# Kernel tuning notes

Hardware: AMD Instinct MI355X
Metric: run time of the kernel (lower is better)

The kernel has to match this reference:

```python
import jax, jax.numpy as jnp
import numpy as np

DIM = 1024; DEPTH = 2; HEADS = 8; DH = DIM // HEADS  # 128
BUCKET = 64; NHASH = 4; MULT = 4
B = 2; T = 4096
NBUCKETS = T // BUCKET  # 64
SCALE = DH ** -0.5
SELF_ATTN_VAL = -5e4  # TOKEN_SELF_ATTN_VALUE in reformer-pytorch
EPS = 1e-5


def layer_norm(x, g, b):
    m = jnp.mean(x, -1, keepdims=True)
    v = jnp.var(x, -1, keepdims=True)
    return (x - m) * jax.lax.rsqrt(v + EPS) * g + b


def lsh_attn(xn, Wqk, Wv, Wo, bo, rot):
    # xn: [B,T,DIM] already layer-normed. Shared-QK LSH attention (reformer-pytorch).
    qk = (xn @ Wqk).reshape(B, T, HEADS, DH).transpose(0, 2, 1, 3).reshape(B * HEADS, T, DH)
    v = (xn @ Wv).reshape(B, T, HEADS, DH).transpose(0, 2, 1, 3).reshape(B * HEADS, T, DH)
    bh = B * HEADS
    # --- hashing with random rotations ---
    rotated = jnp.einsum('btf,fhi->bhti', qk, rot)            # [bh,NHASH,T,NBUCKETS//2]
    rotated = jnp.concatenate([rotated, -rotated], -1)        # [bh,NHASH,T,NBUCKETS]
    buckets = jnp.argmax(rotated, -1)                         # [bh,NHASH,T]
    offs = (jnp.arange(NHASH) * NBUCKETS)[:, None]
    buckets = (buckets + offs).reshape(bh, NHASH * T)
    ticker = jnp.arange(NHASH * T)
    bt = buckets * T + (ticker % T)                           # unique keys -> stable-equivalent sort
    sticker = jnp.argsort(bt, axis=-1)                        # [bh, NHASH*T]
    undo = jnp.argsort(sticker, axis=-1)
    st = sticker % T                                          # original positions, bucket-sorted
    sqk = jnp.take_along_axis(qk, st[..., None], axis=1)
    sv = jnp.take_along_axis(v, st[..., None], axis=1)
    nchunks = NHASH * NBUCKETS
    bq_t = st.reshape(bh, nchunks, BUCKET)
    bqk = sqk.reshape(bh, nchunks, BUCKET, DH)
    bv = sv.reshape(bh, nchunks, BUCKET, DH)
    bq = bqk
    bk = bqk / jnp.clip(jnp.linalg.norm(bqk, axis=-1, keepdims=True), 1e-12)
    def look_one_back(a):
        extra = jnp.concatenate([a[:, -1:], a[:, :-1]], axis=1)
        return jnp.concatenate([a, extra], axis=2)
    bk = look_one_back(bk); bv = look_one_back(bv); bkv_t = look_one_back(bq_t)
    dots = jnp.einsum('bcie,bcje->bcij', bq, bk) * SCALE      # [bh,nchunks,BUCKET,2*BUCKET]
    self_mask = bq_t[..., :, None] == bkv_t[..., None, :]     # shared-QK: penalize i==j
    dots = jnp.where(self_mask, SELF_ATTN_VAL, dots)
    lse = jax.nn.logsumexp(dots, axis=-1, keepdims=True)
    p = jnp.exp(dots - lse)
    bo_ = jnp.einsum('bcij,bcje->bcie', p, bv)
    so = bo_.reshape(bh, NHASH * T, DH)
    slog = lse.reshape(bh, NHASH * T)
    o = jnp.take_along_axis(so, undo[..., None], axis=1)
    logits = jnp.take_along_axis(slog, undo, axis=1)
    o = o.reshape(bh, NHASH, T, DH)
    logits = logits.reshape(bh, NHASH, T, 1)
    probs = jnp.exp(logits - jax.nn.logsumexp(logits, axis=1, keepdims=True))
    out = jnp.sum(o * probs, axis=1)                          # combine hash rounds
    out = out.reshape(B, HEADS, T, DH).transpose(0, 2, 1, 3).reshape(B, T, HEADS * DH)
    return out @ Wo + bo


def setup_inputs() -> dict:
    key = jax.random.key(0)
    ks = jax.random.split(key, 16)
    s = 0.02
    d = {
        'x': jax.random.normal(ks[0], (B, T, DIM), jnp.float32),
        'ln1_g': jnp.ones((DEPTH, DIM), jnp.float32),
        'ln1_b': jnp.zeros((DEPTH, DIM), jnp.float32),
        'Wqk': jax.random.normal(ks[1], (DEPTH, DIM, HEADS * DH), jnp.float32) * s,
        'Wv': jax.random.normal(ks[2], (DEPTH, DIM, HEADS * DH), jnp.float32) * s,
        'Wo': jax.random.normal(ks[3], (DEPTH, HEADS * DH, DIM), jnp.float32) * s,
        'bo': jnp.zeros((DEPTH, DIM), jnp.float32),
        'ln2_g': jnp.ones((DEPTH, DIM), jnp.float32),
        'ln2_b': jnp.zeros((DEPTH, DIM), jnp.float32),
        'W1': jax.random.normal(ks[4], (DEPTH, DIM, DIM * MULT), jnp.float32) * s,
        'b1': jnp.zeros((DEPTH, DIM * MULT), jnp.float32),
        'W2': jax.random.normal(ks[5], (DEPTH, DIM * MULT, DIM), jnp.float32) * s,
        'b2': jnp.zeros((DEPTH, DIM), jnp.float32),
        'rotations': jax.random.normal(ks[6], (DEPTH, DH, NHASH, NBUCKETS // 2), jnp.float32),
    }
    return d


def reference(x, ln1_g, ln1_b, Wqk, Wv, Wo, bo, ln2_g, ln2_b, W1, b1, W2, b2, rotations):
    xx = jnp.concatenate([x, x], -1)  # [B,T,2*DIM] reversible pair
    def step(carry, p):
        g1, be1, wqk, wv, wo, bov, g2, be2, w1, bb1, w2, bb2, rot = p
        x1, x2 = jnp.split(carry, 2, axis=-1)
        y1 = x1 + lsh_attn(layer_norm(x2, g1, be1), wqk, wv, wo, bov, rot)
        h = layer_norm(y1, g2, be2)
        ff = jax.nn.gelu(h @ w1 + bb1, approximate=False) @ w2 + bb2
        y2 = x2 + ff
        return jnp.concatenate([y1, y2], -1), None
    params = (ln1_g, ln1_b, Wqk, Wv, Wo, bo, ln2_g, ln2_b, W1, b1, W2, b2, rotations)
    out, _ = jax.lax.scan(step, xx, params)
    y1, y2 = jnp.split(out, 2, axis=-1)
    return y1 + y2
```

## Files before the change

### kernel.cpp

```cpp
#include <hip/hip_runtime.h>
#include <hip/hip_bf16.h>
#include <cmath>

using bf16 = __hip_bfloat16;
typedef __attribute__((ext_vector_type(8))) short short8;
typedef __attribute__((ext_vector_type(4))) float floatx4;

__device__ __forceinline__ float bu2f(ushort u) { return __uint_as_float((unsigned)u << 16); }
__device__ __forceinline__ ushort f2bu(float f) {
  union { bf16 b; ushort u; } cv; cv.b = __float2bfloat16(f); return cv.u;
}
__device__ __forceinline__ void gl_lds16(const ushort* g, ushort* l) {
  __builtin_amdgcn_global_load_lds((const __attribute__((address_space(1))) unsigned*)g,
                                   (__attribute__((address_space(3))) unsigned*)l, 16, 0, 0);
}
__device__ __forceinline__ float fast_gelu(float x) {
  float z = 0.7978845608028654f * (x + 0.044715f * x * x * x);
  z = fmaxf(fminf(z, 10.f), -10.f);
  float e = __expf(2.f * z);
  float t = (e - 1.f) / (e + 1.f);
  return 0.5f * x * (1.f + t);
}

static constexpr int kT   = 4096;
static constexpr int kDim = 1024;
static constexpr float kScale   = 0.08838834764831845f;
static constexpr float kSelfVal = -5.0e4f;

__device__ __forceinline__ int sane_v(float f) { float a = fabsf(f); return (a > 1e-4f && a < 1e4f) ? 1 : 0; }

__global__ __launch_bounds__(256) void k_detect(const unsigned* __restrict__ x, int* __restrict__ flag) {
  __shared__ int cnt;
  int tid = threadIdx.x;
  if (tid == 0) cnt = 0;
  __syncthreads();
  int my = 0;
  const uint4* p = (const uint4*)x;
  for (int q = 0; q < 16; q++) {
    uint4 u = p[tid * 16 + q];
    my += sane_v(__uint_as_float(u.x << 16)) + sane_v(__uint_as_float(u.x & 0xffff0000u));
    my += sane_v(__uint_as_float(u.y << 16)) + sane_v(__uint_as_float(u.y & 0xffff0000u));
    my += sane_v(__uint_as_float(u.z << 16)) + sane_v(__uint_as_float(u.z & 0xffff0000u));
    my += sane_v(__uint_as_float(u.w << 16)) + sane_v(__uint_as_float(u.w & 0xffff0000u));
  }
  atomicAdd(&cnt, my);
  __syncthreads();
  if (tid == 0) flag[0] = (cnt >= 24576) ? 1 : 0;
}

__global__ __launch_bounds__(256) void k_cvt(const int* __restrict__ flag, const void* __restrict__ src,
                                             ushort* __restrict__ dst, int n) {
  int i = blockIdx.x * 256 + threadIdx.x;
  if (i >= n) return;
  dst[i] = (*flag) ? ((const ushort*)src)[i] : f2bu(((const float*)src)[i]);
}

__global__ __launch_bounds__(256) void k_init_any(const int* __restrict__ flag, const void* __restrict__ x,
                                                  float* __restrict__ x1, float* __restrict__ x2) {
  int i = blockIdx.x * 1024 + threadIdx.x * 4;
  float4 f;
  if (*flag) {
    ushort4 u = *(const ushort4*)((const ushort*)x + i);
    f.x = bu2f(u.x); f.y = bu2f(u.y); f.z = bu2f(u.z); f.w = bu2f(u.w);
  } else {
    f = *(const float4*)((const float*)x + i);
  }
  *(float4*)(x1 + i) = f;
  *(float4*)(x2 + i) = f;
}

__global__ __launch_bounds__(256) void k_final_any(const int* __restrict__ flag, const float* __restrict__ x1,
                                                   const float* __restrict__ x2, void* __restrict__ out) {
  int i = blockIdx.x * 1024 + threadIdx.x * 4;
  float4 a = *(const float4*)(x1 + i);
  float4 b = *(const float4*)(x2 + i);
  float4 s; s.x = a.x + b.x; s.y = a.y + b.y; s.z = a.z + b.z; s.w = a.w + b.w;
  if (*flag) {
    ushort4 u; u.x = f2bu(s.x); u.y = f2bu(s.y); u.z = f2bu(s.z); u.w = f2bu(s.w);
    *(ushort4*)((ushort*)out + i) = u;
  } else {
    *(float4*)((float*)out + i) = s;
  }
}

__global__ __launch_bounds__(256) void k_ln(const float* __restrict__ x, const ushort* __restrict__ g,
                                            const ushort* __restrict__ be, ushort* __restrict__ out) {
  __shared__ float ws[4], ws2[4];
  int row = blockIdx.x, tid = threadIdx.x;
  const float* xr = x + (size_t)row * kDim + tid * 4;
  float4 v = *(const float4*)xr;
  float s  = v.x + v.y + v.z + v.w;
  float s2 = v.x*v.x + v.y*v.y + v.z*v.z + v.w*v.w;
  #pragma unroll
  for (int off = 32; off; off >>= 1) { s += __shfl_down(s, off); s2 += __shfl_down(s2, off); }
  int wave = tid >> 6, lane = tid & 63;
  if (lane == 0) { ws[wave] = s; ws2[wave] = s2; }
  __syncthreads();
  s  = ws[0] + ws[1] + ws[2] + ws[3];
  s2 = ws2[0] + ws2[1] + ws2[2] + ws2[3];
  float mean = s * (1.f/1024.f);
  float var  = fmaxf(s2 * (1.f/1024.f) - mean*mean, 0.f);
  float rstd = rsqrtf(var + 1e-5f);
  int cb = tid * 4;
  ushort* o = out + (size_t)row * kDim + cb;
  o[0] = f2bu((v.x - mean) * rstd * bu2f(g[cb+0]) + bu2f(be[cb+0]));
  o[1] = f2bu((v.y - mean) * rstd * bu2f(g[cb+1]) + bu2f(be[cb+1]));
  o[2] = f2bu((v.z - mean) * rstd * bu2f(g[cb+2]) + bu2f(be[cb+2]));
  o[3] = f2bu((v.w - mean) * rstd * bu2f(g[cb+3]) + bu2f(be[cb+3]));
}

__global__ __launch_bounds__(256) void k_transpose2(const int* __restrict__ flag, const void* __restrict__ src_bf,
                                                    const void* __restrict__ src_f, ushort* __restrict__ out,
                                                    int K, int N) {
  __shared__ ushort tile[32][33];
  int isbf = *flag;
  int nb = blockIdx.x * 32, kb = blockIdx.y * 32;
  int tx = threadIdx.x & 31, ty = threadIdx.x >> 5;
  for (int r = ty; r < 32; r += 8) {
    size_t idx = (size_t)(kb + r) * N + nb + tx;
    tile[r][tx] = isbf ? ((const ushort*)src_bf)[idx] : f2bu(((const float*)src_f)[idx]);
  }
  __syncthreads();
  for (int r = ty; r < 32; r += 8) out[(size_t)(nb + r) * K + kb + tx] = tile[tx][r];
}

__global__ __launch_bounds__(256) void k_rot_t(const ushort* __restrict__ rot, ushort* __restrict__ rotT) {
  int tid = threadIdx.x;
  for (int idx = tid; idx < 16384; idx += 256) {
    int n = idx >> 7, k = idx & 127;
    rotT[idx] = rot[k * 128 + n];
  }
}

template <int MW>
__global__ __launch_bounds__(512, 2) void k_gemm5(const ushort* __restrict__ A, const ushort* __restrict__ Bt,
                                                  const ushort* __restrict__ bias, float* __restrict__ Cf,
                                                  ushort* __restrict__ Cb, ushort* __restrict__ Cb2,
                                                  int M, int N, int K, int mode) {
  constexpr int BM = MW * 32;
  constexpr int LA = MW / 4;
  constexpr int PF = (MW == 8) ? 2 : 3;
  __shared__ alignas(16) ushort SAu[4 * BM * 32];
  __shared__ alignas(16) ushort SBu[4 * 256 * 32];

  const int tid  = threadIdx.x;
  const int lane = tid & 63, wave = tid >> 6;
  const int lr = lane & 15, g = lane >> 4;
  const int wm = wave >> 2, wn = wave & 3;

  const int nbx = gridDim.x;
  const int nwg = nbx * gridDim.y;
  const int bid = blockIdx.y * nbx + blockIdx.x;
  const int swz = (bid & 7) * (nwg >> 3) + (bid >> 3);
  const int m0 = (swz / nbx) * BM;
  const int n0 = (swz % nbx) * 256;

  const int NT = K >> 5;

  const ushort* srcA[LA];
  #pragma unroll
  for (int j = 0; j < LA; j++) {
    int chunk = wave * (64 * LA) + j * 64 + lane;
    int row = chunk >> 2, c = chunk & 3;
    int cs = c ^ ((row >> 1) & 3);
    srcA[j] = A + (size_t)(m0 + row) * K + cs * 8;
  }
  const ushort* srcB[2];
  #pragma unroll
  for (int j = 0; j < 2; j++) {
    int chunk = wave * 128 + j * 64 + lane;
    int row = chunk >> 2, c = chunk & 3;
    int cs = c ^ ((row >> 1) & 3);
    srcB[j] = Bt + (size_t)(n0 + row) * K + cs * 8;
  }

  int offA[MW], offB[4];
  #pragma unroll
  for (int mi = 0; mi < MW; mi++) {
    int row = wm * (MW * 16) + mi * 16 + lr;
    offA[mi] = row * 32 + ((g ^ ((row >> 1) & 3)) * 8);
  }
  #pragma unroll
  for (int ni = 0; ni < 4; ni++) {
    int row = wn * 64 + ni * 16 + lr;
    offB[ni] = row * 32 + ((g ^ ((row >> 1) & 3)) * 8);
  }

  floatx4 acc[MW][4];
  #pragma unroll
  for (int mi = 0; mi < MW; mi++)
    #pragma unroll
    for (int ni = 0; ni < 4; ni++) acc[mi][ni] = (floatx4){0.f, 0.f, 0.f, 0.f};

  #pragma unroll
  for (int p = 0; p < PF; p++) {
    #pragma unroll
    for (int j = 0; j < LA; j++) gl_lds16(srcA[j] + p * 32, SAu + p * (BM * 32) + (wave * (64 * LA) + j * 64) * 8);
    #pragma unroll
    for (int j = 0; j < 2; j++)  gl_lds16(srcB[j] + p * 32, SBu + p * (256 * 32) + (wave * 128 + j * 64) * 8);
  }
  if constexpr (MW == 8) asm volatile("s_waitcnt vmcnt(4)" ::: "memory");
  else                   asm volatile("s_waitcnt vmcnt(6)" ::: "memory");
  __builtin_amdgcn_s_barrier();
  asm volatile("" ::: "memory");

  for (int kt = 0; kt < NT; kt++) {
    const ushort* sa = SAu + (kt & 3) * (BM * 32);
    const ushort* sb = SBu + (kt & 3) * (256 * 32);
    const int kp = ((kt + PF < NT) ? (kt + PF) : 0) * 32;
    const int pb = (kt + PF) & 3;

    short8 a[MW], b[4];
    #pragma unroll
    for (int mi = 0; mi < MW; mi++) a[mi] = *(const short8*)&sa[offA[mi]];
    #pragma unroll
    for (int ni = 0; ni < 4; ni++)  b[ni] = *(const short8*)&sb[offB[ni]];

    #pragma unroll
    for (int j = 0; j < LA; j++) gl_lds16(srcA[j] + kp, SAu + pb * (BM * 32) + (wave * (64 * LA) + j * 64) * 8);
    #pragma unroll
    for (int j = 0; j < 2; j++)  gl_lds16(srcB[j] + kp, SBu + pb * (256 * 32) + (wave * 128 + j * 64) * 8);

    __builtin_amdgcn_s_setprio(1);
    #pragma unroll
    for (int mi = 0; mi < MW; mi++)
      #pragma unroll
      for (int ni = 0; ni < 4; ni++)
        acc[mi][ni] = __builtin_amdgcn_mfma_f32_16x16x32_bf16(a[mi], b[ni], acc[mi][ni], 0, 0, 0);
    __builtin_amdgcn_s_setprio(0);

    if constexpr (MW == 8) asm volatile("s_waitcnt vmcnt(4)" ::: "memory");
    else                   asm volatile("s_waitcnt vmcnt(6)" ::: "memory");
    __builtin_amdgcn_s_barrier();
    asm volatile("" ::: "memory");
  }

  asm volatile("s_waitcnt vmcnt(0)" ::: "memory");
  __syncthreads();

  const int hi4 = (lane >> 4) * 4;

  if (mode == 1) {
    #pragma unroll
    for (int mi = 0; mi < MW; mi++) {
      #pragma unroll
      for (int ni = 0; ni < 4; ni++) {
        int col = n0 + wn * 64 + ni * 16 + lr;
        float bv = bu2f(bias[col]);
        #pragma unroll
        for (int q = 0; q < 4; q++) {
          int r2 = m0 + wm * (MW * 16) + mi * 16 + hi4 + q;
          Cf[(size_t)r2 * N + col] += acc[mi][ni][q] + bv;
        }
      }
    }
  } else {
    ushort* reg0 = (MW == 8) ? SAu : SBu;
    ushort* reg1 = SBu;
    #pragma unroll
    for (int mi = 0; mi < MW; mi++) {
      #pragma unroll
      for (int ni = 0; ni < 4; ni++) {
        int colw = wn * 64 + ni * 16 + lr;
        float bv = (mode == 2) ? bu2f(bias[n0 + colw]) : 0.f;
        #pragma unroll
        for (int q = 0; q < 4; q++) {
          int grow = wm * (MW * 16) + mi * 16 + hi4 + q;
          ushort* reg = (grow < 128) ? reg0 : reg1;
          int rl = grow & 127;
          float val = acc[mi][ni][q];
          ushort h = (mode == 2) ? f2bu(fast_gelu(val + bv)) : f2bu(val);
          reg[rl * 256 + (((colw >> 3) ^ (rl & 7)) * 8) + (colw & 7)] = h;
        }
      }
    }
    __syncthreads();
    {
      const int j = tid & 31;
      const int rsub = tid >> 5;
      #pragma unroll
      for (int p = 0; p < BM / 16; p++) {
        int row = p * 16 + rsub;
        const ushort* reg = (row < 128) ? reg0 : reg1;
        int rl = row & 127;
        short8 v = *(const short8*)&reg[rl * 256 + ((j ^ (rl & 7)) * 8)];
        *(short8*)&Cb[(size_t)(m0 + row) * N + n0 + j * 8] = v;
      }
    }
    if (mode == 5) {
      __syncthreads();
      #pragma unroll
      for (int mi = 0; mi < MW; mi++) {
        #pragma unroll
        for (int ni = 0; ni < 4; ni++) {
          int colw = wn * 64 + ni * 16 + lr;
          #pragma unroll
          for (int q = 0; q < 4; q++) {
            int grow = wm * (MW * 16) + mi * 16 + hi4 + q;
            ushort* reg = (grow < 128) ? reg0 : reg1;
            int rl = grow & 127;
            float val = acc[mi][ni][q];
            ushort h = f2bu(val);
            reg[rl * 256 + (((colw >> 3) ^ (rl & 7)) * 8) + (colw & 7)] = f2bu(val - bu2f(h));
          }
        }
      }
      __syncthreads();
      const int j = tid & 31;
      const int rsub = tid >> 5;
      #pragma unroll
      for (int p = 0; p < BM / 16; p++) {
        int row = p * 16 + rsub;
        const ushort* reg = (row < 128) ? reg0 : reg1;
        int rl = row & 127;
        short8 v = *(const short8*)&reg[rl * 256 + ((j ^ (rl & 7)) * 8)];
        *(short8*)&Cb2[(size_t)(m0 + row) * N + n0 + j * 8] = v;
      }
    }
  }
  (void)M;
}

__global__ __launch_bounds__(256) void k_bucket_mfma(const ushort* __restrict__ qkh, const ushort* __restrict__ qkl,
                                                     const ushort* __restrict__ rotT, int* __restrict__ bkt) {
  __shared__ alignas(16) ushort Bs[128*128];
  __shared__ alignas(16) ushort Ah[64*128];
  __shared__ alignas(16) ushort Al[64*128];
  const int tid = threadIdx.x;
  const int lane = tid & 63, wave = tid >> 6;
  const int lr = lane & 15, lk = (lane >> 4) * 8;
  const int tt = blockIdx.x * 64;
  const int bh = blockIdx.y;
  const int b = bh >> 3, hh = bh & 7;

  {
    int r = tid >> 2, c0 = (tid & 3) * 32;
    size_t base = ((size_t)(b * kT + tt + r)) * kDim + hh * 128 + c0;
    const uint4* sh = (const uint4*)(qkh + base);
    const uint4* sl = (const uint4*)(qkl + base);
    uint4* dh = (uint4*)&Ah[r * 128 + c0];
    uint4* dl = (uint4*)&Al[r * 128 + c0];
    #pragma unroll
    for (int i = 0; i < 4; i++) { dh[i] = sh[i]; dl[i] = sl[i]; }
  }
  {
    const uint4* src = (const uint4*)rotT;
    uint4* dst = (uint4*)Bs;
    for (int i = tid; i < 2048; i += 256) dst[i] = src[i];
  }
  __syncthreads();

  floatx4 acc[4][2];
  #pragma unroll
  for (int mi = 0; mi < 4; mi++) { acc[mi][0] = (floatx4){0,0,0,0}; acc[mi][1] = (floatx4){0,0,0,0}; }
  #pragma unroll
  for (int ks = 0; ks < 4; ks++) {
    short8 a[4], bb[2];
    #pragma unroll
    for (int ni = 0; ni < 2; ni++) bb[ni] = *(const short8*)&Bs[(wave*32 + ni*16 + lr)*128 + ks*32 + lk];
    #pragma unroll
    for (int mi = 0; mi < 4; mi++) a[mi] = *(const short8*)&Ah[(mi*16 + lr)*128 + ks*32 + lk];
    #pragma unroll
    for (int mi = 0; mi < 4; mi++)
      #pragma unroll
      for (int ni = 0; ni < 2; ni++)
        acc[mi][ni] = __builtin_amdgcn_mfma_f32_16x16x32_bf16(a[mi], bb[ni], acc[mi][ni], 0, 0, 0);
  }
  #pragma unroll
  for (int ks = 0; ks < 4; ks++) {
    short8 a[4], bb[2];
    #pragma unroll
    for (int ni = 0; ni < 2; ni++) bb[ni] = *(const short8*)&Bs[(wave*32 + ni*16 + lr)*128 + ks*32 + lk];
    #pragma unroll
    for (int mi = 0; mi < 4; mi++) a[mi] = *(const short8*)&Al[(mi*16 + lr)*128 + ks*32 + lk];
    #pragma unroll
    for (int mi = 0; mi < 4; mi++)
      #pragma unroll
      for (int ni = 0; ni < 2; ni++)
        acc[mi][ni] = __builtin_amdgcn_mfma_f32_16x16x32_bf16(a[mi], bb[ni], acc[mi][ni], 0, 0, 0);
  }

  #pragma unroll
  for (int mi = 0; mi < 4; mi++) {
    #pragma unroll
    for (int q = 0; q < 4; q++) {
      float v0 = acc[mi][0][q];
      float v1 = acc[mi][1][q];
      float best = v0; int bidx = lr;
      if (v1  > best) { best = v1;  bidx = 16 + lr; }
      if (-v0 > best) { best = -v0; bidx = 32 + lr; }
      if (-v1 > best) { best = -v1; bidx = 48 + lr; }
      #pragma unroll
      for (int m = 1; m <= 8; m <<= 1) {
        float ov = __shfl_xor(best, m);
        int   oi = __shfl_xor(bidx, m);
        if (ov > best || (ov == best && oi < bidx)) { best = ov; bidx = oi; }
      }
      if (lr == 0) {
        int row = mi*16 + ((lane >> 4) & 3)*4 + q;
        bkt[(bh*4 + wave)*4096 + tt + row] = bidx;
      }
    }
  }
}

__global__ __launch_bounds__(256) void k_sort(const int* __restrict__ bkt, int* __restrict__ st) {
  __shared__ unsigned char  hist[64*256];
  __shared__ unsigned short offs[64*256];
  __shared__ int base[64];
  int tid = threadIdx.x, grp = blockIdx.x;
  const int* bk = bkt + grp * 4096;
  for (int i = tid; i < 64*256; i += 256) hist[i] = 0;
  __syncthreads();
  int myb[16];
  #pragma unroll
  for (int j = 0; j < 16; j++) {
    myb[j] = bk[tid*16 + j];
    hist[myb[j]*256 + tid] += 1;
  }
  __syncthreads();
  if (tid < 64) {
    int run = 0;
    for (int t = 0; t < 256; t++) { offs[tid*256 + t] = (unsigned short)run; run += hist[tid*256 + t]; }
    base[tid] = run;
  }
  __syncthreads();
  if (tid == 0) {
    int run = 0;
    for (int b2 = 0; b2 < 64; b2++) { int c = base[b2]; base[b2] = run; run += c; }
  }
  __syncthreads();
  #pragma unroll
  for (int j = 0; j < 16; j++) {
    int b2 = myb[j];
    int r = 0;
    for (int jj = 0; jj < j; jj++) r += (myb[jj] == b2) ? 1 : 0;
    st[grp*4096 + base[b2] + (int)offs[b2*256 + tid] + r] = tid*16 + j;
  }
}

__global__ __launch_bounds__(256) void k_attn(const ushort* __restrict__ qkh, const ushort* __restrict__ vbuf,
                                              const int* __restrict__ st, ushort* __restrict__ o_r,
                                              float* __restrict__ lse_r) {
  __shared__ alignas(16) ushort KV[128*136];
  __shared__ alignas(16) ushort Ps[64*136];
  __shared__ float rnorm[128];
  __shared__ int   kposs[128];
  __shared__ float red1[64*4];
  __shared__ float red2[64*4];
  __shared__ float lrow[64];

  const int tid = threadIdx.x;
  const int bid = blockIdx.x;
  const int bh = bid >> 8;
  const int c  = bid & 255;
  const int h  = c >> 6;
  const int cprev = (c + 255) & 255;
  const int b  = bh >> 3, hh = bh & 7;
  const int lane = tid & 63, wave = tid >> 6;
  const int lr = lane & 15, lk = (lane >> 4) * 8;

  {
    int j = tid >> 1, half = tid & 1;
    int slot = (j < 64) ? (c*64 + j) : (cprev*64 + (j - 64));
    int pos = st[bh*16384 + slot];
    if (half == 0) kposs[j] = pos;
    const ushort* src = qkh + ((size_t)(b * kT + pos)) * kDim + hh*128 + half*64;
    float ss = 0.f;
    #pragma unroll
    for (int i2 = 0; i2 < 64; i2 += 8) {
      uint4 u = *(const uint4*)(src + i2);
      *(uint4*)&KV[j*136 + half*64 + i2] = u;
      float f0 = bu2f((ushort)(u.x & 0xffffu)), f1 = bu2f((ushort)(u.x >> 16));
      float f2 = bu2f((ushort)(u.y & 0xffffu)), f3 = bu2f((ushort)(u.y >> 16));
      float f4 = bu2f((ushort)(u.z & 0xffffu)), f5 = bu2f((ushort)(u.z >> 16));
      float f6 = bu2f((ushort)(u.w & 0xffffu)), f7 = bu2f((ushort)(u.w >> 16));
      ss += f0*f0 + f1*f1 + f2*f2 + f3*f3 + f4*f4 + f5*f5 + f6*f6 + f7*f7;
    }
    ss += __shfl_xor(ss, 1);
    if (half == 0) rnorm[j] = 1.f / fmaxf(sqrtf(ss), 1e-12f);
  }
  __syncthreads();

  {
    floatx4 acc[4][2];
    #pragma unroll
    for (int mi = 0; mi < 4; mi++) { acc[mi][0] = (floatx4){0,0,0,0}; acc[mi][1] = (floatx4){0,0,0,0}; }
    #pragma unroll
    for (int ks = 0; ks < 4; ks++) {
      short8 a[4], bb[2];
      #pragma unroll
      for (int mi = 0; mi < 4; mi++) a[mi]  = *(const short8*)&KV[(mi*16 + lr)*136 + ks*32 + lk];
      #pragma unroll
      for (int ni = 0; ni < 2; ni++) bb[ni] = *(const short8*)&KV[(wave*32 + ni*16 + lr)*136 + ks*32 + lk];
      #pragma unroll
      for (int mi = 0; mi < 4; mi++)
        #pragma unroll
        for (int ni = 0; ni < 2; ni++)
          acc[mi][ni] = __builtin_amdgcn_mfma_f32_16x16x32_bf16(a[mi], bb[ni], acc[mi][ni], 0, 0, 0);
    }
    #pragma unroll
    for (int mi = 0; mi < 4; mi++) {
      #pragma unroll
      for (int ni = 0; ni < 2; ni++) {
        int col = wave*32 + ni*16 + lr;
        float rn = rnorm[col] * kScale;
        int cpos = kposs[col];
        #pragma unroll
        for (int q = 0; q < 4; q++) {
          int row = mi*16 + (lane >> 4)*4 + q;
          float val = acc[mi][ni][q] * rn;
          if (cpos == kposs[row]) val = kSelfVal;
          Ps[row*136 + col] = f2bu(val);
        }
      }
    }
  }
  __syncthreads();

  {
    int j = tid >> 1, half = tid & 1;
    int pos = kposs[j];
    const ushort* src = vbuf + ((size_t)(b * kT + pos)) * kDim + hh*128 + half*64;
    #pragma unroll
    for (int i2 = 0; i2 < 64; i2 += 8) {
      uint4 u = *(const uint4*)(src + i2);
      int d0 = half*64 + i2;
      KV[(d0+0)*136 + j] = (ushort)(u.x & 0xffffu); KV[(d0+1)*136 + j] = (ushort)(u.x >> 16);
      KV[(d0+2)*136 + j] = (ushort)(u.y & 0xffffu); KV[(d0+3)*136 + j] = (ushort)(u.y >> 16);
      KV[(d0+4)*136 + j] = (ushort)(u.z & 0xffffu); KV[(d0+5)*136 + j] = (ushort)(u.z >> 16);
      KV[(d0+6)*136 + j] = (ushort)(u.w & 0xffffu); KV[(d0+7)*136 + j] = (ushort)(u.w >> 16);
    }
  }

  {
    int i = tid >> 2, part = tid & 3;
    const int jb = part * 32;
    float m = -1e30f;
    for (int j2 = 0; j2 < 32; j2++) m = fmaxf(m, bu2f(Ps[i*136 + jb + j2]));
    red1[i*4 + part] = m;
    __syncthreads();
    m = fmaxf(fmaxf(red1[i*4+0], red1[i*4+1]), fmaxf(red1[i*4+2], red1[i*4+3]));
    float ssum = 0.f;
    for (int j2 = 0; j2 < 32; j2++) {
      float arg = fmaxf(fminf(bu2f(Ps[i*136 + jb + j2]) - m, 0.f), -80.f);
      float p = __expf(arg);
      ssum += p;
      Ps[i*136 + jb + j2] = f2bu(p);
    }
    red2[i*4 + part] = ssum;
    __syncthreads();
    if (part == 0) {
      float l = fmaxf(red2[i*4+0] + red2[i*4+1] + red2[i*4+2] + red2[i*4+3], 1e-20f);
      lrow[i] = 1.f / l;
      lse_r[(size_t)(bh*4 + h)*4096 + kposs[i]] = m + __logf(l);
    }
  }
  __syncthreads();

  {
    floatx4 acc[4][2];
    #pragma unroll
    for (int mi = 0; mi < 4; mi++) { acc[mi][0] = (floatx4){0,0,0,0}; acc[mi][1] = (floatx4){0,0,0,0}; }
    #pragma unroll
    for (int ks = 0; ks < 4; ks++) {
      short8 a[4], bb[2];
      #pragma unroll
      for (int mi = 0; mi < 4; mi++) a[mi]  = *(const short8*)&Ps[(mi*16 + lr)*136 + ks*32 + lk];
      #pragma unroll
      for (int ni = 0; ni < 2; ni++) bb[ni] = *(const short8*)&KV[(wave*32 + ni*16 + lr)*136 + ks*32 + lk];
      #pragma unroll
      for (int mi = 0; mi < 4; mi++)
        #pragma unroll
        for (int ni = 0; ni < 2; ni++)
          acc[mi][ni] = __builtin_amdgcn_mfma_f32_16x16x32_bf16(a[mi], bb[ni], acc[mi][ni], 0, 0, 0);
    }
    #pragma unroll
    for (int mi = 0; mi < 4; mi++) {
      #pragma unroll
      for (int ni = 0; ni < 2; ni++) {
        int d = wave*32 + ni*16 + lr;
        #pragma unroll
        for (int q = 0; q < 4; q++) {
          int row = mi*16 + (lane >> 4)*4 + q;
          float o = acc[mi][ni][q] * lrow[row];
          o_r[((size_t)(bh*4 + h)*4096 + kposs[row])*128 + d] = f2bu(o);
        }
      }
    }
  }
}

__global__ __launch_bounds__(256) void k_combine(const ushort* __restrict__ o_r, const float* __restrict__ lse_r,
                                                 ushort* __restrict__ attnbf) {
  int rid = blockIdx.x * 2 + (threadIdx.x >> 7);
  int d = threadIdx.x & 127;
  int bh = rid >> 12, t = rid & 4095;
  int b = bh >> 3, hh = bh & 7;
  size_t base = (size_t)bh * 16384 + t;
  float l0 = lse_r[base], l1 = lse_r[base + 4096], l2 = lse_r[base + 8192], l3 = lse_r[base + 12288];
  float M = fmaxf(fmaxf(l0, l1), fmaxf(l2, l3));
  float e0 = __expf(fmaxf(fminf(l0 - M, 0.f), -80.f));
  float e1 = __expf(fmaxf(fminf(l1 - M, 0.f), -80.f));
  float e2 = __expf(fmaxf(fminf(l2 - M, 0.f), -80.f));
  float e3 = __expf(fmaxf(fminf(l3 - M, 0.f), -80.f));
  float inv = 1.f / (e0 + e1 + e2 + e3);
  float o = e0 * bu2f(o_r[(base         )*128 + d]) + e1 * bu2f(o_r[(base +  4096)*128 + d])
          + e2 * bu2f(o_r[(base +  8192)*128 + d]) + e3 * bu2f(o_r[(base + 12288)*128 + d]);
  attnbf[((size_t)b * kT + t) * kDim + hh*128 + d] = f2bu(o * inv);
}

extern "C" void kernel_launch(void* const* d_in, const int* in_sizes, int n_in,
                              void* d_out, int out_size, void* d_ws, size_t ws_size,
                              hipStream_t stream) {
  (void)in_sizes; (void)n_in; (void)out_size; (void)ws_size;
  const void* x     = d_in[0];
  const void* ln1_g = d_in[1];
  const void* ln1_b = d_in[2];
  const void* Wqk   = d_in[3];
  const void* Wv    = d_in[4];
  const void* Wo    = d_in[5];
  const void* bo    = d_in[6];
  const void* ln2_g = d_in[7];
  const void* ln2_b = d_in[8];
  const void* W1    = d_in[9];
  const void* b1    = d_in[10];
  const void* W2    = d_in[11];
  const void* b2    = d_in[12];
  const void* rot   = d_in[13];

  char* w = (char*)d_ws;
  int*    flag = (int*)w;    w += 256;
  ushort* prm  = (ushort*)w; w += 131072;
  float* x1  = (float*)w;  w += 33554432;
  float* x2  = (float*)w;  w += 33554432;
  ushort* qkh = (ushort*)w; w += 16777216;
  ushort* qkl = (ushort*)w; w += 16777216;
  ushort* vbb = (ushort*)w; w += 16777216;
  ushort* xbf = (ushort*)w; w += 16777216;
  ushort* orb = (ushort*)w; w += 67108864;
  float* lse = (float*)w;  w += 1048576;
  int*   bkt = (int*)w;    w += 1048576;
  int*   stb = (int*)w;    w += 1048576;
  ushort* wtA = (ushort*)w; w += 2097152;
  ushort* wtB = (ushort*)w; w += 2097152;
  ushort* wtC = (ushort*)w; w += 2097152;
  ushort* wt1 = (ushort*)w; w += 8388608;
  ushort* wt2 = (ushort*)w; w += 8388608;
  ushort* rtT = (ushort*)w; w += 32768;

  ushort* pLN1G = prm + 0;     ushort* pLN1B = prm + 2048;
  ushort* pBO   = prm + 4096;  ushort* pLN2G = prm + 6144;
  ushort* pLN2B = prm + 8192;  ushort* pB1   = prm + 10240;
  ushort* pB2   = prm + 18432; ushort* pROT  = prm + 20480;

  k_detect<<<1, 256, 0, stream>>>((const unsigned*)x, flag);
  k_cvt<<<8,   256, 0, stream>>>(flag, ln1_g, pLN1G, 2048);
  k_cvt<<<8,   256, 0, stream>>>(flag, ln1_b, pLN1B, 2048);
  k_cvt<<<8,   256, 0, stream>>>(flag, bo,    pBO,   2048);
  k_cvt<<<8,   256, 0, stream>>>(flag, ln2_g, pLN2G, 2048);
  k_cvt<<<8,   256, 0, stream>>>(flag, ln2_b, pLN2B, 2048);
  k_cvt<<<32,  256, 0, stream>>>(flag, b1,    pB1,   8192);
  k_cvt<<<8,   256, 0, stream>>>(flag, b2,    pB2,   2048);
  k_cvt<<<128, 256, 0, stream>>>(flag, rot,   pROT,  32768);
  k_init_any<<<8192, 256, 0, stream>>>(flag, x, x1, x2);

  for (int d = 0; d < 2; d++) {
    k_transpose2<<<dim3(32, 32),  256, 0, stream>>>(flag,
        (const char*)Wqk + (size_t)d*1048576*2, (const char*)Wqk + (size_t)d*1048576*4, wtA, 1024, 1024);
    k_transpose2<<<dim3(32, 32),  256, 0, stream>>>(flag,
        (const char*)Wv  + (size_t)d*1048576*2, (const char*)Wv  + (size_t)d*1048576*4, wtB, 1024, 1024);
    k_transpose2<<<dim3(32, 32),  256, 0, stream>>>(flag,
        (const char*)Wo  + (size_t)d*1048576*2, (const char*)Wo  + (size_t)d*1048576*4, wtC, 1024, 1024);
    k_transpose2<<<dim3(128, 32), 256, 0, stream>>>(flag,
        (const char*)W1  + (size_t)d*4194304*2, (const char*)W1  + (size_t)d*4194304*4, wt1, 1024, 4096);
    k_transpose2<<<dim3(32, 128), 256, 0, stream>>>(flag,
        (const char*)W2  + (size_t)d*4194304*2, (const char*)W2  + (size_t)d*4194304*4, wt2, 4096, 1024);
    k_rot_t<<<1, 256, 0, stream>>>(pROT + (size_t)d * 16384, rtT);

    k_ln<<<8192, 256, 0, stream>>>(x2, pLN1G + d*1024, pLN1B + d*1024, xbf);
    k_gemm5<4><<<dim3(4, 64), 512, 0, stream>>>(xbf, wtA, nullptr, nullptr, qkh, qkl, 8192, 1024, 1024, 5);
    k_gemm5<4><<<dim3(4, 64), 512, 0, stream>>>(xbf, wtB, nullptr, nullptr, vbb, nullptr, 8192, 1024, 1024, 3);
    k_bucket_mfma<<<dim3(64, 16), 256, 0, stream>>>(qkh, qkl, rtT, bkt);
    k_sort<<<64, 256, 0, stream>>>(bkt, stb);
    k_attn<<<4096, 256, 0, stream>>>(qkh, vbb, stb, orb, lse);
    k_combine<<<32768, 256, 0, stream>>>(orb, lse, xbf);
    k_gemm5<4><<<dim3(4, 64), 512, 0, stream>>>(xbf, wtC, pBO + d*1024, x1, nullptr, nullptr, 8192, 1024, 1024, 1);
    k_ln<<<8192, 256, 0, stream>>>(x1, pLN2G + d*1024, pLN2B + d*1024, xbf);
    k_gemm5<8><<<dim3(16, 32), 512, 0, stream>>>(xbf, wt1, pB1 + d*4096, nullptr, orb, nullptr, 8192, 4096, 1024, 2);
    k_gemm5<4><<<dim3(4, 64), 512, 0, stream>>>(orb, wt2, pB2 + d*1024, x2, nullptr, nullptr, 8192, 1024, 4096, 1);
  }
  k_final_any<<<8192, 256, 0, stream>>>(flag, x1, x2, d_out);
}
```

Baseline: 1.108 ms.

## Replace GEMM with 128x128 tile, 256-thread, triple-buffered kernel for all projections

Swaps the templated 512-thread GEMM (128x256 or 256x256 tiles, 4-stage LDS ring) for a single 256-thread kernel with 128x128 tiles and a 3-stage LDS ring, targeting 3 blocks per CU. Smaller tiles give more workgroups and higher occupancy, but each tile is reloaded more often and the per-FLOP load traffic rises. The epilogue staging is remapped to split rows across the two smaller LDS buffers, and the loop adds an explicit lgkmcnt wait before the barrier.

After: 1.108 ms. About the same (-0.0%).

```diff
diff --git a/kernel.cpp b/kernel.cpp
--- a/kernel.cpp
+++ b/kernel.cpp
@@ -132,52 +132,40 @@
   }
 }
 
-template <int MW>
-__global__ __launch_bounds__(512, 2) void k_gemm5(const ushort* __restrict__ A, const ushort* __restrict__ Bt,
+__global__ __launch_bounds__(256, 3) void k_gemm6(const ushort* __restrict__ A, const ushort* __restrict__ Bt,
                                                   const ushort* __restrict__ bias, float* __restrict__ Cf,
                                                   ushort* __restrict__ Cb, ushort* __restrict__ Cb2,
                                                   int M, int N, int K, int mode) {
-  constexpr int BM = MW * 32;
-  constexpr int LA = MW / 4;
-  constexpr int PF = (MW == 8) ? 2 : 3;
-  __shared__ alignas(16) ushort SAu[4 * BM * 32];
-  __shared__ alignas(16) ushort SBu[4 * 256 * 32];
-
+  __shared__ alignas(16) ushort SAu[3 * 128 * 32];
+  __shared__ alignas(16) ushort SBu[3 * 128 * 32];
   const int tid  = threadIdx.x;
   const int lane = tid & 63, wave = tid >> 6;
   const int lr = lane & 15, g = lane >> 4;
-  const int wm = wave >> 2, wn = wave & 3;
+  const int wm = wave >> 1, wn = wave & 1;
 
   const int nbx = gridDim.x;
   const int nwg = nbx * gridDim.y;
   const int bid = blockIdx.y * nbx + blockIdx.x;
   const int swz = (bid & 7) * (nwg >> 3) + (bid >> 3);
-  const int m0 = (swz / nbx) * BM;
-  const int n0 = (swz % nbx) * 256;
-
+  const int m0 = (swz / nbx) * 128;
+  const int n0 = (swz % nbx) * 128;
   const int NT = K >> 5;
 
-  const ushort* srcA[LA];
-  #pragma unroll
-  for (int j = 0; j < LA; j++) {
-    int chunk = wave * (64 * LA) + j * 64 + lane;
-    int row = chunk >> 2, c = chunk & 3;
-    int cs = c ^ ((row >> 1) & 3);
-    srcA[j] = A + (size_t)(m0 + row) * K + cs * 8;
-  }
+  const ushort* srcA[2];
   const ushort* srcB[2];
   #pragma unroll
   for (int j = 0; j < 2; j++) {
     int chunk = wave * 128 + j * 64 + lane;
     int row = chunk >> 2, c = chunk & 3;
     int cs = c ^ ((row >> 1) & 3);
+    srcA[j] = A  + (size_t)(m0 + row) * K + cs * 8;
     srcB[j] = Bt + (size_t)(n0 + row) * K + cs * 8;
   }
 
-  int offA[MW], offB[4];
-  #pragma unroll
-  for (int mi = 0; mi < MW; mi++) {
-    int row = wm * (MW * 16) + mi * 16 + lr;
+  int offA[4], offB[4];
+  #pragma unroll
+  for (int mi = 0; mi < 4; mi++) {
+    int row = wm * 64 + mi * 16 + lr;
     offA[mi] = row * 32 + ((g ^ ((row >> 1) & 3)) * 8);
   }
   #pragma unroll
@@ -186,53 +174,57 @@
     offB[ni] = row * 32 + ((g ^ ((row >> 1) & 3)) * 8);
   }
 
-  floatx4 acc[MW][4];
-  #pragma unroll
-  for (int mi = 0; mi < MW; mi++)
+  floatx4 acc[4][4];
+  #pragma unroll
+  for (int mi = 0; mi < 4; mi++)
     #pragma unroll
     for (int ni = 0; ni < 4; ni++) acc[mi][ni] = (floatx4){0.f, 0.f, 0.f, 0.f};
 
   #pragma unroll
-  for (int p = 0; p < PF; p++) {
-    #pragma unroll
-    for (int j = 0; j < LA; j++) gl_lds16(srcA[j] + p * 32, SAu + p * (BM * 32) + (wave * (64 * LA) + j * 64) * 8);
-    #pragma unroll
-    for (int j = 0; j < 2; j++)  gl_lds16(srcB[j] + p * 32, SBu + p * (256 * 32) + (wave * 128 + j * 64) * 8);
-  }
-  if constexpr (MW == 8) asm volatile("s_waitcnt vmcnt(4)" ::: "memory");
-  else                   asm volatile("s_waitcnt vmcnt(6)" ::: "memory");
+  for (int p = 0; p < 2; p++) {
+    #pragma unroll
+    for (int j = 0; j < 2; j++) {
+      gl_lds16(srcA[j] + p * 32, SAu + p * 4096 + (wave * 128 + j * 64) * 8);
+      gl_lds16(srcB[j] + p * 32, SBu + p * 4096 + (wave * 128 + j * 64) * 8);
+    }
+  }
+  asm volatile("s_waitcnt vmcnt(4)" ::: "memory");
   __builtin_amdgcn_s_barrier();
   asm volatile("" ::: "memory");
 
+  int cur = 0;
   for (int kt = 0; kt < NT; kt++) {
-    const ushort* sa = SAu + (kt & 3) * (BM * 32);
-    const ushort* sb = SBu + (kt & 3) * (256 * 32);
-    const int kp = ((kt + PF < NT) ? (kt + PF) : 0) * 32;
-    const int pb = (kt + PF) & 3;
-
-    short8 a[MW], b[4];
-    #pragma unroll
-    for (int mi = 0; mi < MW; mi++) a[mi] = *(const short8*)&sa[offA[mi]];
-    #pragma unroll
-    for (int ni = 0; ni < 4; ni++)  b[ni] = *(const short8*)&sb[offB[ni]];
-
-    #pragma unroll
-    for (int j = 0; j < LA; j++) gl_lds16(srcA[j] + kp, SAu + pb * (BM * 32) + (wave * (64 * LA) + j * 64) * 8);
-    #pragma unroll
-    for (int j = 0; j < 2; j++)  gl_lds16(srcB[j] + kp, SBu + pb * (256 * 32) + (wave * 128 + j * 64) * 8);
+    const ushort* sa = SAu + cur * 4096;
+    const ushort* sb = SBu + cur * 4096;
+    int pb = cur + 2; if (pb >= 3) pb -= 3;
+    const int kp = ((kt + 2 < NT) ? (kt + 2) : 0) * 32;
+
+    short8 a[4], b[4];
+    #pragma unroll
+    for (int mi = 0; mi < 4; mi++) a[mi] = *(const short8*)&sa[offA[mi]];
+    #pragma unroll
+    for (int ni = 0; ni < 4; ni++) b[ni] = *(const short8*)&sb[offB[ni]];
+
+    #pragma unroll
+    for (int j = 0; j < 2; j++) {
+      gl_lds16(srcA[j] + kp, SAu + pb * 4096 + (wave * 128 + j * 64) * 8);
+      gl_lds16(srcB[j] + kp, SBu + pb * 4096 + (wave * 128 + j * 64) * 8);
+    }
 
     __builtin_amdgcn_s_setprio(1);
     #pragma unroll
-    for (int mi = 0; mi < MW; mi++)
+    for (int mi = 0; mi < 4; mi++)
       #pragma unroll
       for (int ni = 0; ni < 4; ni++)
         acc[mi][ni] = __builtin_amdgcn_mfma_f32_16x16x32_bf16(a[mi], b[ni], acc[mi][ni], 0, 0, 0);
     __builtin_amdgcn_s_setprio(0);
 
-    if constexpr (MW == 8) asm volatile("s_waitcnt vmcnt(4)" ::: "memory");
-    else                   asm volatile("s_waitcnt vmcnt(6)" ::: "memory");
+    asm volatile("s_waitcnt lgkmcnt(0)" ::: "memory");
+    asm volatile("s_waitcnt vmcnt(4)" ::: "memory");
     __builtin_amdgcn_s_barrier();
     asm volatile("" ::: "memory");
+
+    cur = (cur == 2) ? 0 : cur + 1;
   }
 
   asm volatile("s_waitcnt vmcnt(0)" ::: "memory");
@@ -242,78 +234,72 @@
 
   if (mode == 1) {
     #pragma unroll
-    for (int mi = 0; mi < MW; mi++) {
+    for (int mi = 0; mi < 4; mi++) {
       #pragma unroll
       for (int ni = 0; ni < 4; ni++) {
         int col = n0 + wn * 64 + ni * 16 + lr;
         float bv = bu2f(bias[col]);
         #pragma unroll
         for (int q = 0; q < 4; q++) {
-          int r2 = m0 + wm * (MW * 16) + mi * 16 + hi4 + q;
+          int r2 = m0 + wm * 64 + mi * 16 + hi4 + q;
           Cf[(size_t)r2 * N + col] += acc[mi][ni][q] + bv;
         }
       }
     }
   } else {
-    ushort* reg0 = (MW == 8) ? SAu : SBu;
-    ushort* reg1 = SBu;
-    #pragma unroll
-    for (int mi = 0; mi < MW; mi++) {
+    #pragma unroll
+    for (int mi = 0; mi < 4; mi++) {
       #pragma unroll
       for (int ni = 0; ni < 4; ni++) {
         int colw = wn * 64 + ni * 16 + lr;
         float bv = (mode == 2) ? bu2f(bias[n0 + colw]) : 0.f;
         #pragma unroll
         for (int q = 0; q < 4; q++) {
-          int grow = wm * (MW * 16) + mi * 16 + hi4 + q;
-          ushort* reg = (grow < 128) ? reg0 : reg1;
-          int rl = grow & 127;
+          int rl = wm * 64 + mi * 16 + hi4 + q;
+          ushort* rowp = (rl < 96) ? (SBu + rl * 128) : (SAu + (rl - 96) * 128);
           float val = acc[mi][ni][q];
           ushort h = (mode == 2) ? f2bu(fast_gelu(val + bv)) : f2bu(val);
-          reg[rl * 256 + (((colw >> 3) ^ (rl & 7)) * 8) + (colw & 7)] = h;
+          rowp[(((colw >> 3) ^ (rl & 7)) * 8) + (colw & 7)] = h;
         }
       }
     }
     __syncthreads();
     {
-      const int j = tid & 31;
-      const int rsub = tid >> 5;
-      #pragma unroll
-      for (int p = 0; p < BM / 16; p++) {
+      const int j = tid & 15;
+      const int rsub = tid >> 4;
+      #pragma unroll
+      for (int p = 0; p < 8; p++) {
         int row = p * 16 + rsub;
-        const ushort* reg = (row < 128) ? reg0 : reg1;
-        int rl = row & 127;
-        short8 v = *(const short8*)&reg[rl * 256 + ((j ^ (rl & 7)) * 8)];
+        const ushort* rowp = (row < 96) ? (SBu + row * 128) : (SAu + (row - 96) * 128);
+        short8 v = *(const short8*)&rowp[(j ^ (row & 7)) * 8];
         *(short8*)&Cb[(size_t)(m0 + row) * N + n0 + j * 8] = v;
       }
     }
     if (mode == 5) {
       __syncthreads();
       #pragma unroll
-      for (int mi = 0; mi < MW; mi++) {
+      for (int mi = 0; mi < 4; mi++) {
         #pragma unroll
         for (int ni = 0; ni < 4; ni++) {
           int colw = wn * 64 + ni * 16 + lr;
           #pragma unroll
           for (int q = 0; q < 4; q++) {
-            int grow = wm * (MW * 16) + mi * 16 + hi4 + q;
-            ushort* reg = (grow < 128) ? reg0 : reg1;
-            int rl = grow & 127;
+            int rl = wm * 64 + mi * 16 + hi4 + q;
+            ushort* rowp = (rl < 96) ? (SBu + rl * 128) : (SAu + (rl - 96) * 128);
             float val = acc[mi][ni][q];
             ushort h = f2bu(val);
-            reg[rl * 256 + (((colw >> 3) ^ (rl & 7)) * 8) + (colw & 7)] = f2bu(val - bu2f(h));
+            rowp[(((colw >> 3) ^ (rl & 7)) * 8) + (colw & 7)] = f2bu(val - bu2f(h));
           }
         }
       }
       __syncthreads();
-      const int j = tid & 31;
-      const int rsub = tid >> 5;
-      #pragma unroll
-      for (int p = 0; p < BM / 16; p++) {
+      const int j = tid & 15;
+      const int rsub = tid >> 4;
+      #pragma unroll
+      for (int p = 0; p < 8; p++) {
         int row = p * 16 + rsub;
-        const ushort* reg = (row < 128) ? reg0 : reg1;
-        int rl = row & 127;
-        short8 v = *(const short8*)&reg[rl * 256 + ((j ^ (rl & 7)) * 8)];
+        const ushort* rowp = (row < 96) ? (SBu + row * 128) : (SAu + (row - 96) * 128);
+        short8 v = *(const short8*)&rowp[(j ^ (row & 7)) * 8];
         *(short8*)&Cb2[(size_t)(m0 + row) * N + n0 + j * 8] = v;
       }
     }
@@ -679,16 +665,16 @@
     k_rot_t<<<1, 256, 0, stream>>>(pROT + (size_t)d * 16384, rtT);
 
     k_ln<<<8192, 256, 0, stream>>>(x2, pLN1G + d*1024, pLN1B + d*1024, xbf);
-    k_gemm5<4><<<dim3(4, 64), 512, 0, stream>>>(xbf, wtA, nullptr, nullptr, qkh, qkl, 8192, 1024, 1024, 5);
-    k_gemm5<4><<<dim3(4, 64), 512, 0, stream>>>(xbf, wtB, nullptr, nullptr, vbb, nullptr, 8192, 1024, 1024, 3);
+    k_gemm6<<<dim3(8, 64), 256, 0, stream>>>(xbf, wtA, nullptr, nullptr, qkh, qkl, 8192, 1024, 1024, 5);
+    k_gemm6<<<dim3(8, 64), 256, 0, stream>>>(xbf, wtB, nullptr, nullptr, vbb, nullptr, 8192, 1024, 1024, 3);
     k_bucket_mfma<<<dim3(64, 16), 256, 0, stream>>>(qkh, qkl, rtT, bkt);
     k_sort<<<64, 256, 0, stream>>>(bkt, stb);
     k_attn<<<4096, 256, 0, stream>>>(qkh, vbb, stb, orb, lse);
     k_combine<<<32768, 256, 0, stream>>>(orb, lse, xbf);
-    k_gemm5<4><<<dim3(4, 64), 512, 0, stream>>>(xbf, wtC, pBO + d*1024, x1, nullptr, nullptr, 8192, 1024, 1024, 1);
+    k_gemm6<<<dim3(8, 64), 256, 0, stream>>>(xbf, wtC, pBO + d*1024, x1, nullptr, nullptr, 8192, 1024, 1024, 1);
     k_ln<<<8192, 256, 0, stream>>>(x1, pLN2G + d*1024, pLN2B + d*1024, xbf);
-    k_gemm5<8><<<dim3(16, 32), 512, 0, stream>>>(xbf, wt1, pB1 + d*4096, nullptr, orb, nullptr, 8192, 4096, 1024, 2);
-    k_gemm5<4><<<dim3(4, 64), 512, 0, stream>>>(orb, wt2, pB2 + d*1024, x2, nullptr, nullptr, 8192, 1024, 4096, 1);
+    k_gemm6<<<dim3(32, 64), 256, 0, stream>>>(xbf, wt1, pB1 + d*4096, nullptr, orb, nullptr, 8192, 4096, 1024, 2);
+    k_gemm6<<<dim3(8, 64), 256, 0, stream>>>(orb, wt2, pB2 + d*1024, x2, nullptr, nullptr, 8192, 1024, 4096, 1);
   }
   k_final_any<<<8192, 256, 0, stream>>>(flag, x1, x2, d_out);
 }
```
